# Performance work log

Measured on AMD Instinct MI355X. Metric: run time of the kernel, lower is better.

Reference implementation:

```python
import jax, jax.numpy as jnp
import numpy as np

ANG = 9        # angRes (forced by hardcoded center index 40 -> 81 views)
MINDISP = -4
MAXDISP = 4


def setup_inputs() -> dict:
    key = jax.random.key(0)
    k1, k2 = jax.random.split(key)
    x = jax.random.normal(k1, (2, 4, 81, 96, 96), dtype=jnp.float32)
    mask = jax.random.uniform(k2, (2, 81, 96, 96), dtype=jnp.float32)
    return {"x": x, "mask": mask}


def _build_cost(x, mask):
    # Faithful translation of BuildCost.forward.
    # The chain of (ZeroPad2d on each view) -> (macro-image rearrange) ->
    # (crop) -> (Unfold kernel=A, dilation=(h_pad-d, w_pad-d)) -> (mask
    # modulate) -> (Unfold2) is algebraically a per-view shifted gather:
    #   cost[b,d,p,q,ck,u,v] = x_padview[b,ck,u,v, p+off(d,u), q+off(d,v)]
    #                          * mask[b, u*A+v, p, q]
    # with off(d,t) = (A//2)*(d-mindisp) - t*d, on views zero-padded by
    # bdr = (A//2)*maxdisp. Unfold2 is a pure reshape of the modulated
    # unfold columns. All indices stay inside each padded view.
    A, mind, maxd = ANG, MINDISP, MAXDISP
    b, c, aa, h, w = x.shape
    ctr = x[:, :, 40:41, :, :]                       # [b, c, 1, h, w]
    c0 = A // 2
    bdr = c0 * maxd
    xv = x.reshape(b, c, A, A, h, w)
    xp = jnp.pad(xv, ((0, 0), (0, 0), (0, 0), (0, 0), (bdr, bdr), (bdr, bdr)))
    D = maxd - mind + 1
    d = jnp.arange(mind, maxd + 1)                   # [D]
    uv = jnp.arange(A)                               # [A]
    off = c0 * (d[:, None] - mind) - uv[None, :] * d[:, None]   # [D, A]
    ridx = off[:, :, None] + jnp.arange(h)[None, None, :]       # [D, A, h]
    cidx = off[:, :, None] + jnp.arange(w)[None, None, :]       # [D, A, w]
    ui = uv[None, :, None, None, None]               # broadcast to [D,A,A,h,w]
    vi = uv[None, None, :, None, None]
    ri = ridx[:, :, None, :, None]
    ci = cidx[:, None, :, None, :]
    # g[b, c, D, u, v, p, q]
    g = xp[:, :, ui, vi, ri, ci]
    m = mask.reshape(b, 1, 1, A, A, h, w)            # mask channel a = u*A+v
    cost = g * m
    # torch output layout: [b, D, (p*w+q)*c + ck, u*A+v]
    cost = cost.transpose(0, 2, 5, 6, 1, 3, 4).reshape(b, D, h * w * c, A * A)
    return cost, ctr


def reference(x, mask):
    return _build_cost(x, mask)
```

## Files before the change

### kernel.cpp

```cpp
#include <hip/hip_runtime.h>


#define NAA 81
#define H 96
#define W 96
#define NC 4
#define ND 9
#define PLANE 9216
#define NR 324
#define JB 32
#define OUTROW 31104
#define CTR_OFF 53747712LL
#define XTOT 5971968

typedef float f32x4 __attribute__((ext_vector_type(4)));
typedef f32x4 __attribute__((aligned(4))) f32x4u;

__global__ __launch_bounds__(512, 6)
void build_cost_kernel(const float* __restrict__ x, const float* __restrict__ mask,
                       float* __restrict__ out) {
    __shared__ __align__(16) float xs[JB * NR];
    __shared__ __align__(16) int   lut[2 * NR];

    const int D   = blockIdx.x;
    const int xcd = D & 7;
    const int s_  = D >> 3;
    const int b   = s_ / 324;
    const int w_  = s_ - 324 * b;
    const int dd  = w_ / 36;
    const int r_  = w_ - 36 * dd;
    const int jc  = r_ / 12;
    const int iio = r_ - 12 * jc;
    const int ii  = 12 * xcd + iio;
    const int j0  = JB * jc;
    const int d   = dd - 4;
    const int tid = threadIdx.x;

    if (tid < NR) {
        int row = tid;
        int c  = row / 81;
        int uv = row - 81 * c;
        int u  = uv / 9;
        int v  = uv - 9 * u;
        int ri = ii + d * (4 - u);
        int xb = ((b * NC + c) * NAA + uv) * PLANE + ri * W;
        int mb = ((b * NAA + uv) * H + ii) * W;
        int s  = d * (4 - v);
        lut[2 * tid]     = ((unsigned)ri < (unsigned)H) ? xb : -1;
        lut[2 * tid + 1] = (mb << 6) | (s + 16);
    }
    __syncthreads();

    for (int idx = tid; idx < NAA * 8; idx += 512) {
        int rq = idx >> 3;
        int j4 = idx & 7;
        int jb = 4 * j4;
        int4 P0 = *(const int4*)&lut[8 * rq];
        int4 P1 = *(const int4*)&lut[8 * rq + 4];

        auto ld = [&](int xb, int B) -> f32x4 {
            int s    = (B & 63) - 16;
            int col0 = j0 + jb + s;
            int a0   = xb + col0;
            int addr = min(max(a0, 0), XTOT - 4);
            f32x4 xv = *(const f32x4u*)(x + addr);
            f32x4 mv = *(const f32x4*)(mask + (B >> 6) + j0 + jb);
            f32x4 r;
            bool rv = (xb >= 0);
            r.x = (rv && (unsigned)(col0 + 0) < (unsigned)W) ? xv.x * mv.x : 0.0f;
            r.y = (rv && (unsigned)(col0 + 1) < (unsigned)W) ? xv.y * mv.y : 0.0f;
            r.z = (rv && (unsigned)(col0 + 2) < (unsigned)W) ? xv.z * mv.z : 0.0f;
            r.w = (rv && (unsigned)(col0 + 3) < (unsigned)W) ? xv.w * mv.w : 0.0f;
            return r;
        };

        f32x4 v0 = ld(P0.x, P0.y);
        f32x4 v1 = ld(P0.z, P0.w);
        f32x4 v2 = ld(P1.x, P1.y);
        f32x4 v3 = ld(P1.z, P1.w);

        float* base = &xs[4 * rq];
        f32x4 w0 = {v0.x, v1.x, v2.x, v3.x};
        f32x4 w1 = {v0.y, v1.y, v2.y, v3.y};
        f32x4 w2 = {v0.z, v1.z, v2.z, v3.z};
        f32x4 w3 = {v0.w, v1.w, v2.w, v3.w};
        *(f32x4*)(base + (jb + 0) * NR) = w0;
        *(f32x4*)(base + (jb + 1) * NR) = w1;
        *(f32x4*)(base + (jb + 2) * NR) = w2;
        *(f32x4*)(base + (jb + 3) * NR) = w3;
    }
    __syncthreads();

    const size_t obase = (size_t)((b * ND + dd) * H + ii) * OUTROW + (size_t)j0 * NR;
    for (int idx = tid; idx < NAA * JB; idx += 512) {
        f32x4 v = *(const f32x4*)&xs[4 * idx];
        __builtin_nontemporal_store(v, (f32x4*)(out + obase + 4 * (size_t)idx));
    }

    if (dd == 4 && jc == 0 && tid < 96) {
        int c = tid / 24;
        int q = tid - 24 * c;
        size_t so  = (size_t)((b * NC + c) * NAA + 40) * PLANE + (size_t)ii * W + 4 * q;
        size_t dst = CTR_OFF + (size_t)((b * NC + c) * H + ii) * W + 4 * q;
        f32x4 cv = *(const f32x4*)(x + so);
        __builtin_nontemporal_store(cv, (f32x4*)(out + dst));
    }
}

extern "C" void kernel_launch(void* const* d_in, const int* in_sizes, int n_in,
                              void* d_out, int out_size, void* d_ws, size_t ws_size,
                              hipStream_t stream) {
    const float* x    = (const float*)d_in[0];
    const float* mask = (const float*)d_in[1];
    float* out = (float*)d_out;
    dim3 grid(5184, 1, 1);
    build_cost_kernel<<<grid, 512, 0, stream>>>(x, mask, out);
}
```

Measured before the change: 241.6 us.

## Double-buffer LDS subtiles so each block handles a full output row

Each block now covers a whole 96-column output row, processed as six 16-column subtiles through two LDS buffers, instead of one 32-column chunk per block. Gathers for the next subtile are issued before the current subtile is stored, overlapping global loads with nontemporal stores, and the LUT is built once per row instead of three times. The grid shrinks threefold, which lowers parallelism, and the barrier now waits only on LDS counters.

```diff
diff --git a/kernel.cpp b/kernel.cpp
--- a/kernel.cpp
+++ b/kernel.cpp
@@ -8,7 +8,9 @@
 #define ND 9
 #define PLANE 9216
 #define NR 324
-#define JB 32
+#define SUB 16
+#define NSUB 6
+#define SUBV (SUB * NR / 4)
 #define OUTROW 31104
 #define CTR_OFF 53747712LL
 #define XTOT 5971968
@@ -16,23 +18,36 @@
 typedef float f32x4 __attribute__((ext_vector_type(4)));
 typedef f32x4 __attribute__((aligned(4))) f32x4u;
 
+#define BAR() do { \
+    asm volatile("s_waitcnt lgkmcnt(0)" ::: "memory"); \
+    __builtin_amdgcn_s_barrier(); \
+} while (0)
+
+__device__ __forceinline__ f32x4 combine(f32x4 xv, f32x4 mv, int xb, int col0) {
+    f32x4 r;
+    bool rv = xb >= 0;
+    r.x = (rv && (unsigned)(col0 + 0) < (unsigned)W) ? xv.x * mv.x : 0.0f;
+    r.y = (rv && (unsigned)(col0 + 1) < (unsigned)W) ? xv.y * mv.y : 0.0f;
+    r.z = (rv && (unsigned)(col0 + 2) < (unsigned)W) ? xv.z * mv.z : 0.0f;
+    r.w = (rv && (unsigned)(col0 + 3) < (unsigned)W) ? xv.w * mv.w : 0.0f;
+    return r;
+}
+
 __global__ __launch_bounds__(512, 6)
 void build_cost_kernel(const float* __restrict__ x, const float* __restrict__ mask,
                        float* __restrict__ out) {
-    __shared__ __align__(16) float xs[JB * NR];
+    __shared__ __align__(16) float xs0[SUB * NR];
+    __shared__ __align__(16) float xs1[SUB * NR];
     __shared__ __align__(16) int   lut[2 * NR];
 
     const int D   = blockIdx.x;
     const int xcd = D & 7;
     const int s_  = D >> 3;
-    const int b   = s_ / 324;
-    const int w_  = s_ - 324 * b;
-    const int dd  = w_ / 36;
-    const int r_  = w_ - 36 * dd;
-    const int jc  = r_ / 12;
-    const int iio = r_ - 12 * jc;
+    const int b   = s_ / 108;
+    const int w_  = s_ - 108 * b;
+    const int dd  = w_ / 12;
+    const int iio = w_ - 12 * dd;
     const int ii  = 12 * xcd + iio;
-    const int j0  = JB * jc;
     const int d   = dd - 4;
     const int tid = threadIdx.x;
 
@@ -49,61 +64,83 @@
         lut[2 * tid]     = ((unsigned)ri < (unsigned)H) ? xb : -1;
         lut[2 * tid + 1] = (mb << 6) | (s + 16);
     }
-    __syncthreads();
+    BAR();
 
-    for (int idx = tid; idx < NAA * 8; idx += 512) {
-        int rq = idx >> 3;
-        int j4 = idx & 7;
-        int jb = 4 * j4;
-        int4 P0 = *(const int4*)&lut[8 * rq];
-        int4 P1 = *(const int4*)&lut[8 * rq + 4];
-
-        auto ld = [&](int xb, int B) -> f32x4 {
-            int s    = (B & 63) - 16;
-            int col0 = j0 + jb + s;
-            int a0   = xb + col0;
-            int addr = min(max(a0, 0), XTOT - 4);
-            f32x4 xv = *(const f32x4u*)(x + addr);
-            f32x4 mv = *(const f32x4*)(mask + (B >> 6) + j0 + jb);
-            f32x4 r;
-            bool rv = (xb >= 0);
-            r.x = (rv && (unsigned)(col0 + 0) < (unsigned)W) ? xv.x * mv.x : 0.0f;
-            r.y = (rv && (unsigned)(col0 + 1) < (unsigned)W) ? xv.y * mv.y : 0.0f;
-            r.z = (rv && (unsigned)(col0 + 2) < (unsigned)W) ? xv.z * mv.z : 0.0f;
-            r.w = (rv && (unsigned)(col0 + 3) < (unsigned)W) ? xv.w * mv.w : 0.0f;
-            return r;
-        };
-
-        f32x4 v0 = ld(P0.x, P0.y);
-        f32x4 v1 = ld(P0.z, P0.w);
-        f32x4 v2 = ld(P1.x, P1.y);
-        f32x4 v3 = ld(P1.z, P1.w);
-
-        float* base = &xs[4 * rq];
-        f32x4 w0 = {v0.x, v1.x, v2.x, v3.x};
-        f32x4 w1 = {v0.y, v1.y, v2.y, v3.y};
-        f32x4 w2 = {v0.z, v1.z, v2.z, v3.z};
-        f32x4 w3 = {v0.w, v1.w, v2.w, v3.w};
-        *(f32x4*)(base + (jb + 0) * NR) = w0;
-        *(f32x4*)(base + (jb + 1) * NR) = w1;
-        *(f32x4*)(base + (jb + 2) * NR) = w2;
-        *(f32x4*)(base + (jb + 3) * NR) = w3;
-    }
-    __syncthreads();
-
-    const size_t obase = (size_t)((b * ND + dd) * H + ii) * OUTROW + (size_t)j0 * NR;
-    for (int idx = tid; idx < NAA * JB; idx += 512) {
-        f32x4 v = *(const f32x4*)&xs[4 * idx];
-        __builtin_nontemporal_store(v, (f32x4*)(out + obase + 4 * (size_t)idx));
-    }
-
-    if (dd == 4 && jc == 0 && tid < 96) {
+    if (dd == 4 && tid < 96) {
         int c = tid / 24;
         int q = tid - 24 * c;
         size_t so  = (size_t)((b * NC + c) * NAA + 40) * PLANE + (size_t)ii * W + 4 * q;
         size_t dst = CTR_OFF + (size_t)((b * NC + c) * H + ii) * W + 4 * q;
         f32x4 cv = *(const f32x4*)(x + so);
         __builtin_nontemporal_store(cv, (f32x4*)(out + dst));
+    }
+
+    const bool active = tid < 4 * NAA;
+    const int rq = tid >> 2;
+    const int jb = (tid & 3) * 4;
+    int4 P0, P1;
+    if (active) {
+        P0 = *(const int4*)&lut[8 * rq];
+        P1 = *(const int4*)&lut[8 * rq + 4];
+    }
+
+    f32x4 xr0, xr1, xr2, xr3;
+
+    auto issue = [&](int j0) {
+        xr0 = *(const f32x4u*)(x + min(max(P0.x + j0 + jb + ((P0.y & 63) - 16), 0), XTOT - 4));
+        xr1 = *(const f32x4u*)(x + min(max(P0.z + j0 + jb + ((P0.w & 63) - 16), 0), XTOT - 4));
+        xr2 = *(const f32x4u*)(x + min(max(P1.x + j0 + jb + ((P1.y & 63) - 16), 0), XTOT - 4));
+        xr3 = *(const f32x4u*)(x + min(max(P1.z + j0 + jb + ((P1.w & 63) - 16), 0), XTOT - 4));
+    };
+
+    auto combine_write = [&](int j0, float* buf) {
+        f32x4 m0 = *(const f32x4*)(mask + (P0.y >> 6) + j0 + jb);
+        f32x4 m1 = *(const f32x4*)(mask + (P0.w >> 6) + j0 + jb);
+        f32x4 m2 = *(const f32x4*)(mask + (P1.y >> 6) + j0 + jb);
+        f32x4 m3 = *(const f32x4*)(mask + (P1.w >> 6) + j0 + jb);
+        f32x4 v0 = combine(xr0, m0, P0.x, j0 + jb + ((P0.y & 63) - 16));
+        f32x4 v1 = combine(xr1, m1, P0.z, j0 + jb + ((P0.w & 63) - 16));
+        f32x4 v2 = combine(xr2, m2, P1.x, j0 + jb + ((P1.y & 63) - 16));
+        f32x4 v3 = combine(xr3, m3, P1.z, j0 + jb + ((P1.w & 63) - 16));
+        float* bp = buf + 4 * rq + jb * NR;
+        f32x4 t0 = {v0.x, v1.x, v2.x, v3.x};
+        f32x4 t1 = {v0.y, v1.y, v2.y, v3.y};
+        f32x4 t2 = {v0.z, v1.z, v2.z, v3.z};
+        f32x4 t3 = {v0.w, v1.w, v2.w, v3.w};
+        *(f32x4*)(bp + 0 * NR) = t0;
+        *(f32x4*)(bp + 1 * NR) = t1;
+        *(f32x4*)(bp + 2 * NR) = t2;
+        *(f32x4*)(bp + 3 * NR) = t3;
+    };
+
+    const size_t obase = (size_t)((b * ND + dd) * H + ii) * OUTROW;
+
+    auto store_sub = [&](int k, const float* sp) {
+        const size_t cb = obase + (size_t)(SUB * k) * NR;
+        #pragma unroll
+        for (int m = 0; m < 2; ++m) {
+            int idx = tid + 512 * m;
+            f32x4 v = *(const f32x4*)(sp + 4 * idx);
+            __builtin_nontemporal_store(v, (f32x4*)(out + cb + 4 * (size_t)idx));
+        }
+        if (tid < SUBV - 1024) {
+            int idx = tid + 1024;
+            f32x4 v = *(const f32x4*)(sp + 4 * idx);
+            __builtin_nontemporal_store(v, (f32x4*)(out + cb + 4 * (size_t)idx));
+        }
+    };
+
+    if (active) { issue(0); combine_write(0, xs0); }
+    BAR();
+
+    #pragma unroll
+    for (int k = 0; k < NSUB; ++k) {
+        float* rbuf = (k & 1) ? xs1 : xs0;
+        float* wbuf = (k & 1) ? xs0 : xs1;
+        if (k < NSUB - 1 && active) issue(SUB * (k + 1));
+        store_sub(k, rbuf);
+        if (k < NSUB - 1 && active) combine_write(SUB * (k + 1), wbuf);
+        BAR();
     }
 }
 
@@ -113,6 +150,6 @@
     const float* x    = (const float*)d_in[0];
     const float* mask = (const float*)d_in[1];
     float* out = (float*)d_out;
-    dim3 grid(5184, 1, 1);
+    dim3 grid(1728, 1, 1);
     build_cost_kernel<<<grid, 512, 0, stream>>>(x, mask, out);
 }
```

Result: slower. 261.8 us (+8.4%).

## Process three disparities per block and cache mask tile in shared memory

Applied to the files above, without the earlier changes.

Each block now handles three disparity values instead of one, cutting the grid to a third, and stages the mask tile into shared memory once for reuse across the three passes. The per-block index lookup table is dropped and indices are recomputed inline. This is meant to reduce redundant mask loads and per-block setup. The cost is fewer blocks, a serialized loop with extra barriers per block, and more integer arithmetic per element in a kernel that is bound by output writes.

```diff
diff --git a/kernel.cpp b/kernel.cpp
--- a/kernel.cpp
+++ b/kernel.cpp
@@ -20,90 +20,86 @@
 void build_cost_kernel(const float* __restrict__ x, const float* __restrict__ mask,
                        float* __restrict__ out) {
     __shared__ __align__(16) float xs[JB * NR];
-    __shared__ __align__(16) int   lut[2 * NR];
+    __shared__ __align__(16) float ms[NAA * JB];
 
     const int D   = blockIdx.x;
     const int xcd = D & 7;
     const int s_  = D >> 3;
-    const int b   = s_ / 324;
-    const int w_  = s_ - 324 * b;
-    const int dd  = w_ / 36;
-    const int r_  = w_ - 36 * dd;
+    const int b   = s_ / 108;
+    const int w_  = s_ - 108 * b;
+    const int ddg = w_ / 36;
+    const int r_  = w_ - 36 * ddg;
     const int jc  = r_ / 12;
     const int iio = r_ - 12 * jc;
     const int ii  = 12 * xcd + iio;
     const int j0  = JB * jc;
-    const int d   = dd - 4;
     const int tid = threadIdx.x;
 
-    if (tid < NR) {
-        int row = tid;
-        int c  = row / 81;
-        int uv = row - 81 * c;
-        int u  = uv / 9;
-        int v  = uv - 9 * u;
-        int ri = ii + d * (4 - u);
-        int xb = ((b * NC + c) * NAA + uv) * PLANE + ri * W;
-        int mb = ((b * NAA + uv) * H + ii) * W;
-        int s  = d * (4 - v);
-        lut[2 * tid]     = ((unsigned)ri < (unsigned)H) ? xb : -1;
-        lut[2 * tid + 1] = (mb << 6) | (s + 16);
-    }
-    __syncthreads();
-
     for (int idx = tid; idx < NAA * 8; idx += 512) {
-        int rq = idx >> 3;
+        int uv = idx >> 3;
         int j4 = idx & 7;
-        int jb = 4 * j4;
-        int4 P0 = *(const int4*)&lut[8 * rq];
-        int4 P1 = *(const int4*)&lut[8 * rq + 4];
-
-        auto ld = [&](int xb, int B) -> f32x4 {
-            int s    = (B & 63) - 16;
-            int col0 = j0 + jb + s;
-            int a0   = xb + col0;
-            int addr = min(max(a0, 0), XTOT - 4);
-            f32x4 xv = *(const f32x4u*)(x + addr);
-            f32x4 mv = *(const f32x4*)(mask + (B >> 6) + j0 + jb);
-            f32x4 r;
-            bool rv = (xb >= 0);
-            r.x = (rv && (unsigned)(col0 + 0) < (unsigned)W) ? xv.x * mv.x : 0.0f;
-            r.y = (rv && (unsigned)(col0 + 1) < (unsigned)W) ? xv.y * mv.y : 0.0f;
-            r.z = (rv && (unsigned)(col0 + 2) < (unsigned)W) ? xv.z * mv.z : 0.0f;
-            r.w = (rv && (unsigned)(col0 + 3) < (unsigned)W) ? xv.w * mv.w : 0.0f;
-            return r;
-        };
-
-        f32x4 v0 = ld(P0.x, P0.y);
-        f32x4 v1 = ld(P0.z, P0.w);
-        f32x4 v2 = ld(P1.x, P1.y);
-        f32x4 v3 = ld(P1.z, P1.w);
-
-        float* base = &xs[4 * rq];
-        f32x4 w0 = {v0.x, v1.x, v2.x, v3.x};
-        f32x4 w1 = {v0.y, v1.y, v2.y, v3.y};
-        f32x4 w2 = {v0.z, v1.z, v2.z, v3.z};
-        f32x4 w3 = {v0.w, v1.w, v2.w, v3.w};
-        *(f32x4*)(base + (jb + 0) * NR) = w0;
-        *(f32x4*)(base + (jb + 1) * NR) = w1;
-        *(f32x4*)(base + (jb + 2) * NR) = w2;
-        *(f32x4*)(base + (jb + 3) * NR) = w3;
-    }
-    __syncthreads();
-
-    const size_t obase = (size_t)((b * ND + dd) * H + ii) * OUTROW + (size_t)j0 * NR;
-    for (int idx = tid; idx < NAA * JB; idx += 512) {
-        f32x4 v = *(const f32x4*)&xs[4 * idx];
-        __builtin_nontemporal_store(v, (f32x4*)(out + obase + 4 * (size_t)idx));
+        f32x4 mv = *(const f32x4*)(mask + ((b * NAA + uv) * H + ii) * W + j0 + 4 * j4);
+        *(f32x4*)&ms[uv * JB + 4 * j4] = mv;
     }
 
-    if (dd == 4 && jc == 0 && tid < 96) {
+    if (ddg == 1 && jc == 0 && tid < 96) {
         int c = tid / 24;
         int q = tid - 24 * c;
         size_t so  = (size_t)((b * NC + c) * NAA + 40) * PLANE + (size_t)ii * W + 4 * q;
         size_t dst = CTR_OFF + (size_t)((b * NC + c) * H + ii) * W + 4 * q;
         f32x4 cv = *(const f32x4*)(x + so);
         __builtin_nontemporal_store(cv, (f32x4*)(out + dst));
+    }
+    __syncthreads();
+
+    #pragma unroll
+    for (int pass = 0; pass < 3; ++pass) {
+        const int dd = 3 * ddg + pass;
+        const int d  = dd - 4;
+
+        for (int idx = tid; idx < NAA * 8; idx += 512) {
+            int rq = idx >> 3;
+            int j4 = idx & 7;
+            int jb = 4 * j4;
+            f32x4 v[4];
+            #pragma unroll
+            for (int r = 0; r < 4; ++r) {
+                int row = 4 * rq + r;
+                int c   = row / 81;
+                int uv  = row - 81 * c;
+                int u   = uv / 9;
+                int vv  = uv - 9 * u;
+                int ri  = ii + d * (4 - u);
+                int s   = d * (4 - vv);
+                int col0 = j0 + jb + s;
+                int xb  = ((b * NC + c) * NAA + uv) * PLANE + ri * W;
+                int addr = min(max(xb + col0, 0), XTOT - 4);
+                f32x4 xv = *(const f32x4u*)(x + addr);
+                f32x4 mv = *(const f32x4*)&ms[uv * JB + jb];
+                bool rv  = (unsigned)ri < (unsigned)H;
+                v[r].x = (rv && (unsigned)(col0 + 0) < (unsigned)W) ? xv.x * mv.x : 0.0f;
+                v[r].y = (rv && (unsigned)(col0 + 1) < (unsigned)W) ? xv.y * mv.y : 0.0f;
+                v[r].z = (rv && (unsigned)(col0 + 2) < (unsigned)W) ? xv.z * mv.z : 0.0f;
+                v[r].w = (rv && (unsigned)(col0 + 3) < (unsigned)W) ? xv.w * mv.w : 0.0f;
+            }
+            float* base = &xs[4 * rq];
+            f32x4 w0 = {v[0].x, v[1].x, v[2].x, v[3].x};
+            f32x4 w1 = {v[0].y, v[1].y, v[2].y, v[3].y};
+            f32x4 w2 = {v[0].z, v[1].z, v[2].z, v[3].z};
+            f32x4 w3 = {v[0].w, v[1].w, v[2].w, v[3].w};
+            *(f32x4*)(base + (jb + 0) * NR) = w0;
+            *(f32x4*)(base + (jb + 1) * NR) = w1;
+            *(f32x4*)(base + (jb + 2) * NR) = w2;
+            *(f32x4*)(base + (jb + 3) * NR) = w3;
+        }
+        __syncthreads();
+
+        const size_t obase = (size_t)((b * ND + dd) * H + ii) * OUTROW + (size_t)j0 * NR;
+        for (int idx = tid; idx < NAA * JB; idx += 512) {
+            f32x4 v = *(const f32x4*)&xs[4 * idx];
+            __builtin_nontemporal_store(v, (f32x4*)(out + obase + 4 * (size_t)idx));
+        }
+        __syncthreads();
     }
 }
 
@@ -113,6 +109,6 @@
     const float* x    = (const float*)d_in[0];
     const float* mask = (const float*)d_in[1];
     float* out = (float*)d_out;
-    dim3 grid(5184, 1, 1);
+    dim3 grid(1728, 1, 1);
     build_cost_kernel<<<grid, 512, 0, stream>>>(x, mask, out);
 }
```

Measured after the change: 237.5 us. No clear change (-1.7%).
